# Kernel optimization log

Measured on AMD Instinct MI355X. Metric: run time of the kernel, lower is better.

## Reference

```python
import jax, jax.numpy as jnp
import numpy as np

N = 50000
E = 600000
IN1, IN2, HID, OUT = 256, 128, 128, 64


def gcn_conv(x, W, b, src, dst, n):
    """PyG GCNConv: D^{-1/2}(A+I)D^{-1/2} X W + b with self-loops."""
    h = x @ W  # [N, F_out]
    # degree including self-loop (edge weight 1)
    deg = jax.ops.segment_sum(jnp.ones_like(dst, dtype=h.dtype), dst, num_segments=n) + 1.0
    dinv = deg ** -0.5
    coef = dinv[src] * dinv[dst]  # [E]
    agg = jax.ops.segment_sum(h[src] * coef[:, None], dst, num_segments=n)
    agg = agg + h * (dinv * dinv)[:, None]  # self-loop contribution
    return agg + b


def gcn_stack(x, edge_index, Ws, bs, n):
    src, dst = edge_index[0], edge_index[1]
    x = jax.nn.relu(gcn_conv(x, Ws[0], bs[0], src, dst, n))
    return gcn_conv(x, Ws[1], bs[1], src, dst, n)


def setup_inputs() -> dict:
    key = jax.random.key(0)
    ks = jax.random.split(key, 12)
    glorot = lambda k, fi, fo: jax.random.normal(k, (fi, fo), jnp.float32) * np.sqrt(2.0 / (fi + fo))
    return {
        "x1": jax.random.normal(ks[0], (N, IN1), jnp.float32),
        "edge_index1": jax.random.randint(ks[1], (2, E), 0, N, jnp.int32),
        "x2": jax.random.normal(ks[2], (N, IN2), jnp.float32),
        "edge_index2": jax.random.randint(ks[3], (2, E), 0, N, jnp.int32),
        "W1_0": glorot(ks[4], IN1, HID), "b1_0": jnp.zeros((HID,), jnp.float32),
        "W1_1": glorot(ks[5], HID, OUT), "b1_1": jnp.zeros((OUT,), jnp.float32),
        "W2_0": glorot(ks[6], IN2, HID), "b2_0": jnp.zeros((HID,), jnp.float32),
        "W2_1": glorot(ks[7], HID, OUT), "b2_1": jnp.zeros((OUT,), jnp.float32),
    }


def reference(x1, edge_index1, x2, edge_index2,
              W1_0, b1_0, W1_1, b1_1, W2_0, b2_0, W2_1, b2_1):
    out1 = gcn_stack(x1, edge_index1, (W1_0, W1_1), (b1_0, b1_1), N)
    out2 = gcn_stack(x2, edge_index2, (W2_0, W2_1), (b2_0, b2_1), N)
    return out1, out2
```

## Files before the change

kernel.cpp:

```cpp
#include <hip/hip_runtime.h>
#include <hip/hip_bf16.h>
#include <cstdint>
#include <type_traits>

static constexpr int NN = 50000;
static constexpr int NE = 600000;
static constexpr int NB = (NN + 255) / 256;
static constexpr int CHUNK = 1024;
static constexpr int NCH = (NE + CHUNK - 1) / CHUNK;
static constexpr int CAP = 4096;

typedef __bf16 bf16;
typedef __attribute__((ext_vector_type(2))) __bf16 bf16x2;
typedef __attribute__((ext_vector_type(8))) __bf16 bf16x8;
typedef __attribute__((ext_vector_type(4))) float f32x4;

__global__ __launch_bounds__(256) void k_init(int* __restrict__ bucketcur,
                                              int* __restrict__ row_off) {
    int i = blockIdx.x * 256 + threadIdx.x;
    if (i < 2 * NB) bucketcur[i] = i * CAP;
    if (i < 2) row_off[i * (NN + 1) + NN] = NE;
}

__global__ __launch_bounds__(256) void k_binA(const int* __restrict__ srcA,
                                              const int* __restrict__ dstA,
                                              const int* __restrict__ srcB,
                                              const int* __restrict__ dstB,
                                              int* __restrict__ bucketcur,
                                              int2* __restrict__ stg) {
    __shared__ int cnt[NB];
    __shared__ int ibase[NB];
    int g = blockIdx.y;
    const int* src = g ? srcB : srcA;
    const int* dst = g ? dstB : dstA;
    int tid = threadIdx.x;
    int c0 = blockIdx.x * CHUNK;
    if (tid < NB) cnt[tid] = 0;
    __syncthreads();
    #pragma unroll
    for (int it = 0; it < CHUNK / 256; ++it) {
        int e = c0 + it * 256 + tid;
        if (e < NE) atomicAdd(&cnt[dst[e] >> 8], 1);
    }
    __syncthreads();
    if (tid < NB) {
        int c = cnt[tid];
        ibase[tid] = c ? atomicAdd(&bucketcur[g * NB + tid], c) : 0;
        cnt[tid] = 0;
    }
    __syncthreads();
    #pragma unroll
    for (int it = 0; it < CHUNK / 256; ++it) {
        int e = c0 + it * 256 + tid;
        if (e < NE) {
            int s = src[e], d = dst[e];
            int b = d >> 8;
            int p = atomicAdd(&cnt[b], 1);
            stg[(size_t)ibase[b] + p] = make_int2(s, d);
        }
    }
}

__global__ __launch_bounds__(256) void k_bucket_scan(const int* __restrict__ bucketcur,
                                                     int* __restrict__ bucket_base) {
    __shared__ int s[256];
    int g = blockIdx.x;
    int tid = threadIdx.x;
    int B = g * NB + tid;
    int v = (tid < NB) ? bucketcur[B] - B * CAP : 0;
    s[tid] = v;
    __syncthreads();
    for (int off = 1; off < 256; off <<= 1) {
        int t = (tid >= off) ? s[tid - off] : 0;
        __syncthreads();
        s[tid] += t;
        __syncthreads();
    }
    if (tid < NB) bucket_base[B] = s[tid] - v;
}

__global__ __launch_bounds__(256) void k_binB1(const int2* __restrict__ stg,
                                               const int* __restrict__ bucketcur,
                                               const int* __restrict__ bucket_base,
                                               int* __restrict__ row_off,
                                               float* __restrict__ dinv) {
    __shared__ int cnt[256];
    __shared__ int s[256];
    int g = blockIdx.y;
    int b = blockIdx.x;
    int B = g * NB + b;
    int tid = threadIdx.x;
    int node0 = b << 8;
    int nnod = min(256, NN - node0);
    cnt[tid] = 0;
    __syncthreads();
    int count = bucketcur[B] - B * CAP;
    const int2* s0 = stg + (size_t)B * CAP;
    for (int j = tid; j < count; j += 256)
        atomicAdd(&cnt[s0[j].y - node0], 1);
    __syncthreads();
    int v = cnt[tid];
    s[tid] = v;
    __syncthreads();
    for (int off = 1; off < 256; off <<= 1) {
        int t = (tid >= off) ? s[tid - off] : 0;
        __syncthreads();
        s[tid] += t;
        __syncthreads();
    }
    if (tid < nnod) {
        row_off[g * (NN + 1) + node0 + tid] = bucket_base[B] + s[tid] - v;
        dinv[(size_t)g * NN + node0 + tid] = rsqrtf((float)v + 1.0f);
    }
}

__global__ __launch_bounds__(256) void k_binB2(const int2* __restrict__ stg,
                                               const int* __restrict__ bucketcur,
                                               const int* __restrict__ row_off,
                                               const float* __restrict__ dinv,
                                               int2* __restrict__ pair) {
    __shared__ int lcur[256];
    __shared__ float ldv[256];
    int g = blockIdx.y;
    int b = blockIdx.x;
    int B = g * NB + b;
    int tid = threadIdx.x;
    int node0 = b << 8;
    int nnod = min(256, NN - node0);
    const int* ro = row_off + g * (NN + 1);
    if (tid < nnod) {
        lcur[tid] = ro[node0 + tid];
        ldv[tid] = dinv[(size_t)g * NN + node0 + tid];
    }
    __syncthreads();
    int count = bucketcur[B] - B * CAP;
    const int2* s0 = stg + (size_t)B * CAP;
    for (int j = tid; j < count; j += 256) {
        int2 sd = s0[j];
        int rel = sd.y - node0;
        int pos = atomicAdd(&lcur[rel], 1);
        float cf = dinv[(size_t)g * NN + sd.x] * ldv[rel];
        pair[(size_t)g * NE + pos] = make_int2(sd.x, __float_as_int(cf));
    }
}

__global__ __launch_bounds__(256) void k_wprep4(const float* __restrict__ WA,
                                                const float* __restrict__ WB,
                                                const float* __restrict__ WC,
                                                const float* __restrict__ WD,
                                                bf16* __restrict__ wf0,
                                                bf16* __restrict__ wf1) {
    int y = blockIdx.y;
    const float* W = (y == 0) ? WA : (y == 1) ? WB : (y == 2) ? WC : WD;
    bf16* wf = (y == 0) ? wf0 : (y == 1) ? wf0 + 256 * 128 : (y == 2) ? wf1 : wf1 + 128 * 64;
    int K = (y == 0) ? 256 : 128;
    int F = (y <= 1) ? 128 : 64;
    int i = blockIdx.x * 256 + threadIdx.x;
    if (i < K * F) {
        int k = i / F, n = i % F;
        wf[((size_t)(k >> 3) * F + n) * 8 + (k & 7)] = (bf16)W[i];
    }
}

template <int K, int F, typename AT>
__device__ __forceinline__ void gemm_body(const AT* __restrict__ X,
                                          const bf16* __restrict__ wf,
                                          bf16* __restrict__ H, int n, int bx) {
    constexpr int NT = F / 16;
    int wave = threadIdx.x >> 6;
    int lane = threadIdx.x & 63;
    int lm = lane & 15;
    int lk = lane >> 4;
    int r0 = bx * 64 + wave * 16;

    int arow = r0 + lm;
    if (arow >= n) arow = n - 1;
    const AT* xrow = X + (size_t)arow * K;

    f32x4 acc[NT] = {};

    for (int k0 = 0; k0 < K; k0 += 32) {
        bf16x8 af;
        if constexpr (std::is_same_v<AT, float>) {
            f32x4 a0 = *reinterpret_cast<const f32x4*>(xrow + k0 + lk * 8);
            f32x4 a1 = *reinterpret_cast<const f32x4*>(xrow + k0 + lk * 8 + 4);
            af[0] = (bf16)a0.x; af[1] = (bf16)a0.y; af[2] = (bf16)a0.z; af[3] = (bf16)a0.w;
            af[4] = (bf16)a1.x; af[5] = (bf16)a1.y; af[6] = (bf16)a1.z; af[7] = (bf16)a1.w;
        } else {
            af = *reinterpret_cast<const bf16x8*>(xrow + k0 + lk * 8);
        }
        const bf16* wbase = wf + ((size_t)(k0 / 8 + lk) * F) * 8;
        #pragma unroll
        for (int t = 0; t < NT; ++t) {
            bf16x8 bfg = *reinterpret_cast<const bf16x8*>(wbase + (t * 16 + lm) * 8);
            acc[t] = __builtin_amdgcn_mfma_f32_16x16x32_bf16(af, bfg, acc[t], 0, 0, 0);
        }
    }

    #pragma unroll
    for (int t = 0; t < NT; ++t) {
        #pragma unroll
        for (int i = 0; i < 4; ++i) {
            int gr = r0 + lk * 4 + i;
            if (gr < n) H[(size_t)gr * F + t * 16 + lm] = (bf16)acc[t][i];
        }
    }
}

static constexpr int GB = (NN + 63) / 64;

__global__ __launch_bounds__(256) void gemm_l1(const float* __restrict__ x1,
                                               const float* __restrict__ x2,
                                               const bf16* __restrict__ wf0,
                                               bf16* __restrict__ h) {
    int bx = blockIdx.x;
    if (bx < GB)
        gemm_body<256, 128, float>(x1, wf0, h, NN, bx);
    else
        gemm_body<128, 128, float>(x2, wf0 + 256 * 128, h + (size_t)NN * 128, NN, bx - GB);
}

__global__ __launch_bounds__(256) void gemm_l2(const bf16* __restrict__ a,
                                               const bf16* __restrict__ wf1,
                                               bf16* __restrict__ h2) {
    int bx = blockIdx.x;
    int g = (bx >= GB);
    gemm_body<128, 64, bf16>(a + (size_t)g * NN * 128, wf1 + g * 128 * 64,
                             h2 + (size_t)g * NN * 64, NN, bx - g * GB);
}

__global__ __launch_bounds__(256) void agg128_2(const bf16* __restrict__ hb,
                                                const int* __restrict__ row_off,
                                                const int2* __restrict__ pairb,
                                                const float* __restrict__ dinv,
                                                const float* __restrict__ biasA,
                                                const float* __restrict__ biasB,
                                                bf16* __restrict__ ab) {
    int wid = blockIdx.x * 4 + (threadIdx.x >> 6);
    if (wid >= 2 * NN) return;
    int g = (wid >= NN);
    int node = wid - g * NN;
    int lane = threadIdx.x & 63;

    const bf16* h = hb + (size_t)g * NN * 128;
    const int2* pair = pairb + (size_t)g * NE;
    const int* ro = row_off + g * (NN + 1);
    const float* bias = g ? biasB : biasA;

    int f = lane * 2;
    float di = dinv[g * NN + node];
    int beg = ro[node];
    int end = ro[node + 1];

    float a0 = 0.f, a1 = 0.f;

    auto edge1 = [&](int2 p) {
        float c = __int_as_float(p.y);
        bf16x2 v = *reinterpret_cast<const bf16x2*>(&h[(size_t)p.x * 128 + f]);
        a0 = fmaf((float)v[0], c, a0); a1 = fmaf((float)v[1], c, a1);
    };
    auto edge2 = [&](int4 q) {
        float cA = __int_as_float(q.y), cB = __int_as_float(q.w);
        bf16x2 vA = *reinterpret_cast<const bf16x2*>(&h[(size_t)q.x * 128 + f]);
        bf16x2 vB = *reinterpret_cast<const bf16x2*>(&h[(size_t)q.z * 128 + f]);
        a0 = fmaf((float)vA[0], cA, a0); a1 = fmaf((float)vA[1], cA, a1);
        a0 = fmaf((float)vB[0], cB, a0); a1 = fmaf((float)vB[1], cB, a1);
    };

    int j = beg;
    if ((j & 1) && j < end) { edge1(pair[j]); ++j; }
    for (; j + 7 < end; j += 8) {
        int4 q0 = *reinterpret_cast<const int4*>(&pair[j]);
        int4 q1 = *reinterpret_cast<const int4*>(&pair[j + 2]);
        int4 q2 = *reinterpret_cast<const int4*>(&pair[j + 4]);
        int4 q3 = *reinterpret_cast<const int4*>(&pair[j + 6]);
        edge2(q0); edge2(q1); edge2(q2); edge2(q3);
    }
    for (; j + 1 < end; j += 2) {
        int4 q = *reinterpret_cast<const int4*>(&pair[j]);
        edge2(q);
    }
    if (j < end) edge1(pair[j]);

    bf16x2 hv = *reinterpret_cast<const bf16x2*>(&h[(size_t)node * 128 + f]);
    float sc = di * di;
    a0 = fmaf((float)hv[0], sc, a0) + bias[f];
    a1 = fmaf((float)hv[1], sc, a1) + bias[f + 1];
    a0 = fmaxf(a0, 0.f);
    a1 = fmaxf(a1, 0.f);

    bf16x2 r;
    r[0] = (bf16)a0; r[1] = (bf16)a1;
    *reinterpret_cast<bf16x2*>(&ab[((size_t)g * NN + node) * 128 + f]) = r;
}

__global__ __launch_bounds__(256) void agg64_2(const bf16* __restrict__ h2b,
                                               const int* __restrict__ row_off,
                                               const int2* __restrict__ pairb,
                                               const float* __restrict__ dinv,
                                               const float* __restrict__ biasA,
                                               const float* __restrict__ biasB,
                                               float* __restrict__ outb) {
    int wid = blockIdx.x * 4 + (threadIdx.x >> 6);
    if (wid >= 2 * NN) return;
    int g = (wid >= NN);
    int node = wid - g * NN;
    int lane = threadIdx.x & 63;

    const bf16* h = h2b + (size_t)g * NN * 64;
    const int2* pair = pairb + (size_t)g * NE;
    const int* ro = row_off + g * (NN + 1);
    const float* bias = g ? biasB : biasA;
    float* out = outb + (size_t)g * NN * 64;

    int half = lane >> 5;
    int f = (lane & 31) * 2;
    float di = dinv[(size_t)g * NN + node];
    int beg = ro[node];
    int end = ro[node + 1];

    float a0 = 0.f, a1 = 0.f;

    auto edge = [&](int2 p) {
        float c = __int_as_float(p.y);
        bf16x2 v = *reinterpret_cast<const bf16x2*>(&h[(size_t)p.x * 64 + f]);
        a0 = fmaf((float)v[0], c, a0); a1 = fmaf((float)v[1], c, a1);
    };

    int j = beg;
    for (; j + 7 < end; j += 8) {
        int2 p0 = pair[j + half], p1 = pair[j + 2 + half];
        int2 p2 = pair[j + 4 + half], p3 = pair[j + 6 + half];
        edge(p0); edge(p1); edge(p2); edge(p3);
    }
    for (; j + 1 < end; j += 2) edge(pair[j + half]);
    if (j < end && half == 0) edge(pair[j]);

    a0 += __shfl_xor(a0, 32);
    a1 += __shfl_xor(a1, 32);

    bf16x2 hv = *reinterpret_cast<const bf16x2*>(&h[(size_t)node * 64 + f]);
    float sc = di * di;
    a0 = fmaf((float)hv[0], sc, a0) + bias[f];
    a1 = fmaf((float)hv[1], sc, a1) + bias[f + 1];

    if (half == 0) {
        out[(size_t)node * 64 + f] = a0;
        out[(size_t)node * 64 + f + 1] = a1;
    }
}

extern "C" void kernel_launch(void* const* d_in, const int* in_sizes, int n_in,
                              void* d_out, int out_size, void* d_ws, size_t ws_size,
                              hipStream_t stream) {
    const float* x1 = (const float*)d_in[0];
    const int* ei1 = (const int*)d_in[1];
    const float* x2 = (const float*)d_in[2];
    const int* ei2 = (const int*)d_in[3];
    const float* W1_0 = (const float*)d_in[4];
    const float* b1_0 = (const float*)d_in[5];
    const float* W1_1 = (const float*)d_in[6];
    const float* b1_1 = (const float*)d_in[7];
    const float* W2_0 = (const float*)d_in[8];
    const float* b2_0 = (const float*)d_in[9];
    const float* W2_1 = (const float*)d_in[10];
    const float* b2_1 = (const float*)d_in[11];

    float* out = (float*)d_out;

    char* ws = (char*)d_ws;
    size_t off = 0;
    auto alloc = [&](size_t bytes) {
        size_t o = off;
        off = (off + bytes + 255) & ~(size_t)255;
        return o;
    };
    bf16* h = (bf16*)(ws + alloc((size_t)2 * NN * 128 * 2));
    size_t r2 = (size_t)2 * NB * CAP * 8;
    char* region2 = ws + alloc(r2);
    int2* stg = (int2*)region2;
    bf16* h2 = (bf16*)region2;
    bf16* a = (bf16*)(ws + alloc((size_t)2 * NN * 128 * 2));
    int2* pair = (int2*)(ws + alloc((size_t)2 * NE * 8));
    int* row_off = (int*)(ws + alloc((size_t)2 * (NN + 1) * 4));
    float* dinv = (float*)(ws + alloc((size_t)2 * NN * 4));
    int* bucketcur = (int*)(ws + alloc((size_t)2 * NB * 4));
    int* bucket_base = (int*)(ws + alloc((size_t)2 * NB * 4));
    bf16* wf0 = (bf16*)(ws + alloc((size_t)2 * 256 * 128 * 2));
    bf16* wf1 = (bf16*)(ws + alloc((size_t)2 * 128 * 64 * 2));

    const int* srcA = ei1, *dstA = ei1 + NE;
    const int* srcB = ei2, *dstB = ei2 + NE;

    k_init<<<(2 * NB + 255) / 256, 256, 0, stream>>>(bucketcur, row_off);
    k_wprep4<<<dim3(128, 4), 256, 0, stream>>>(W1_0, W2_0, W1_1, W2_1, wf0, wf1);
    k_binA<<<dim3(NCH, 2), 256, 0, stream>>>(srcA, dstA, srcB, dstB, bucketcur, stg);
    k_bucket_scan<<<2, 256, 0, stream>>>(bucketcur, bucket_base);
    k_binB1<<<dim3(NB, 2), 256, 0, stream>>>(stg, bucketcur, bucket_base, row_off, dinv);
    k_binB2<<<dim3(NB, 2), 256, 0, stream>>>(stg, bucketcur, row_off, dinv, pair);

    gemm_l1<<<2 * GB, 256, 0, stream>>>(x1, x2, wf0, h);
    agg128_2<<<(2 * NN + 3) / 4, 256, 0, stream>>>(h, row_off, pair, dinv, b1_0, b2_0, a);
    gemm_l2<<<2 * GB, 256, 0, stream>>>(a, wf1, h2);
    agg64_2<<<(2 * NN + 3) / 4, 256, 0, stream>>>(h2, row_off, pair, dinv, b1_1, b2_1, out);
}
```

Before: 201.7 us.

## Split edges across half-waves in agg128, use nontemporal pair loads, fuse init kernel

The 128-wide aggregation now gives each half-wave alternating edges, with 4 features per lane and 8-byte gathers, and combines the two halves with a cross-half shuffle. This mirrors the existing agg64 scheme and halves the per-lane edge count. Edge pair loads in both aggregation kernels use nontemporal hints so streaming metadata is kept out of cache in favour of the gathered features. The separate init kernel is folded into the weight-prep kernel as an extra grid row, saving one launch. The costs are shuffle overhead and only half the lanes writing the output.

```diff
diff --git a/kernel.cpp b/kernel.cpp
--- a/kernel.cpp
+++ b/kernel.cpp
@@ -12,15 +12,11 @@
 
 typedef __bf16 bf16;
 typedef __attribute__((ext_vector_type(2))) __bf16 bf16x2;
+typedef __attribute__((ext_vector_type(4))) __bf16 bf16x4;
 typedef __attribute__((ext_vector_type(8))) __bf16 bf16x8;
 typedef __attribute__((ext_vector_type(4))) float f32x4;
-
-__global__ __launch_bounds__(256) void k_init(int* __restrict__ bucketcur,
-                                              int* __restrict__ row_off) {
-    int i = blockIdx.x * 256 + threadIdx.x;
-    if (i < 2 * NB) bucketcur[i] = i * CAP;
-    if (i < 2) row_off[i * (NN + 1) + NN] = NE;
-}
+typedef __attribute__((ext_vector_type(2))) int i32x2;
+typedef __attribute__((ext_vector_type(4))) int i32x4;
 
 __global__ __launch_bounds__(256) void k_binA(const int* __restrict__ srcA,
                                               const int* __restrict__ dstA,
@@ -149,13 +145,20 @@
                                                 const float* __restrict__ WC,
                                                 const float* __restrict__ WD,
                                                 bf16* __restrict__ wf0,
-                                                bf16* __restrict__ wf1) {
+                                                bf16* __restrict__ wf1,
+                                                int* __restrict__ bucketcur,
+                                                int* __restrict__ row_off) {
     int y = blockIdx.y;
+    int i = blockIdx.x * 256 + threadIdx.x;
+    if (y == 4) {
+        if (i < 2 * NB) bucketcur[i] = i * CAP;
+        if (i < 2) row_off[i * (NN + 1) + NN] = NE;
+        return;
+    }
     const float* W = (y == 0) ? WA : (y == 1) ? WB : (y == 2) ? WC : WD;
     bf16* wf = (y == 0) ? wf0 : (y == 1) ? wf0 + 256 * 128 : (y == 2) ? wf1 : wf1 + 128 * 64;
     int K = (y == 0) ? 256 : 128;
     int F = (y <= 1) ? 128 : 64;
-    int i = blockIdx.x * 256 + threadIdx.x;
     if (i < K * F) {
         int k = i / F, n = i % F;
         wf[((size_t)(k >> 3) * F + n) * 8 + (k & 7)] = (bf16)W[i];
@@ -241,57 +244,67 @@
     int g = (wid >= NN);
     int node = wid - g * NN;
     int lane = threadIdx.x & 63;
+    int half = lane >> 5;
+    int f = (lane & 31) * 4;
 
     const bf16* h = hb + (size_t)g * NN * 128;
     const int2* pair = pairb + (size_t)g * NE;
     const int* ro = row_off + g * (NN + 1);
     const float* bias = g ? biasB : biasA;
 
-    int f = lane * 2;
     float di = dinv[g * NN + node];
     int beg = ro[node];
     int end = ro[node + 1];
 
-    float a0 = 0.f, a1 = 0.f;
-
-    auto edge1 = [&](int2 p) {
-        float c = __int_as_float(p.y);
-        bf16x2 v = *reinterpret_cast<const bf16x2*>(&h[(size_t)p.x * 128 + f]);
+    float a0 = 0.f, a1 = 0.f, a2 = 0.f, a3 = 0.f;
+
+    auto edge = [&](int s, float c) {
+        bf16x4 v = *reinterpret_cast<const bf16x4*>(&h[(size_t)s * 128 + f]);
         a0 = fmaf((float)v[0], c, a0); a1 = fmaf((float)v[1], c, a1);
+        a2 = fmaf((float)v[2], c, a2); a3 = fmaf((float)v[3], c, a3);
     };
-    auto edge2 = [&](int4 q) {
-        float cA = __int_as_float(q.y), cB = __int_as_float(q.w);
-        bf16x2 vA = *reinterpret_cast<const bf16x2*>(&h[(size_t)q.x * 128 + f]);
-        bf16x2 vB = *reinterpret_cast<const bf16x2*>(&h[(size_t)q.z * 128 + f]);
-        a0 = fmaf((float)vA[0], cA, a0); a1 = fmaf((float)vA[1], cA, a1);
-        a0 = fmaf((float)vB[0], cB, a0); a1 = fmaf((float)vB[1], cB, a1);
+    auto edge2 = [&](i32x4 q) {
+        int s = half ? q[2] : q[0];
+        float c = __int_as_float(half ? q[3] : q[1]);
+        edge(s, c);
     };
 
     int j = beg;
-    if ((j & 1) && j < end) { edge1(pair[j]); ++j; }
+    if ((j & 1) && j < end) {
+        if (half == 0) { int2 p = pair[j]; edge(p.x, __int_as_float(p.y)); }
+        ++j;
+    }
     for (; j + 7 < end; j += 8) {
-        int4 q0 = *reinterpret_cast<const int4*>(&pair[j]);
-        int4 q1 = *reinterpret_cast<const int4*>(&pair[j + 2]);
-        int4 q2 = *reinterpret_cast<const int4*>(&pair[j + 4]);
-        int4 q3 = *reinterpret_cast<const int4*>(&pair[j + 6]);
+        i32x4 q0 = __builtin_nontemporal_load(reinterpret_cast<const i32x4*>(&pair[j]));
+        i32x4 q1 = __builtin_nontemporal_load(reinterpret_cast<const i32x4*>(&pair[j + 2]));
+        i32x4 q2 = __builtin_nontemporal_load(reinterpret_cast<const i32x4*>(&pair[j + 4]));
+        i32x4 q3 = __builtin_nontemporal_load(reinterpret_cast<const i32x4*>(&pair[j + 6]));
         edge2(q0); edge2(q1); edge2(q2); edge2(q3);
     }
     for (; j + 1 < end; j += 2) {
-        int4 q = *reinterpret_cast<const int4*>(&pair[j]);
+        i32x4 q = __builtin_nontemporal_load(reinterpret_cast<const i32x4*>(&pair[j]));
         edge2(q);
     }
-    if (j < end) edge1(pair[j]);
-
-    bf16x2 hv = *reinterpret_cast<const bf16x2*>(&h[(size_t)node * 128 + f]);
+    if (j < end && half == 0) { int2 p = pair[j]; edge(p.x, __int_as_float(p.y)); }
+
+    a0 += __shfl_xor(a0, 32);
+    a1 += __shfl_xor(a1, 32);
+    a2 += __shfl_xor(a2, 32);
+    a3 += __shfl_xor(a3, 32);
+
+    bf16x4 hv = *reinterpret_cast<const bf16x4*>(&h[(size_t)node * 128 + f]);
+    f32x4 bv = *reinterpret_cast<const f32x4*>(&bias[f]);
     float sc = di * di;
-    a0 = fmaf((float)hv[0], sc, a0) + bias[f];
-    a1 = fmaf((float)hv[1], sc, a1) + bias[f + 1];
-    a0 = fmaxf(a0, 0.f);
-    a1 = fmaxf(a1, 0.f);
-
-    bf16x2 r;
-    r[0] = (bf16)a0; r[1] = (bf16)a1;
-    *reinterpret_cast<bf16x2*>(&ab[((size_t)g * NN + node) * 128 + f]) = r;
+    a0 = fmaxf(fmaf((float)hv[0], sc, a0) + bv.x, 0.f);
+    a1 = fmaxf(fmaf((float)hv[1], sc, a1) + bv.y, 0.f);
+    a2 = fmaxf(fmaf((float)hv[2], sc, a2) + bv.z, 0.f);
+    a3 = fmaxf(fmaf((float)hv[3], sc, a3) + bv.w, 0.f);
+
+    if (half == 0) {
+        bf16x4 r;
+        r[0] = (bf16)a0; r[1] = (bf16)a1; r[2] = (bf16)a2; r[3] = (bf16)a3;
+        *reinterpret_cast<bf16x4*>(&ab[((size_t)g * NN + node) * 128 + f]) = r;
+    }
 }
 
 __global__ __launch_bounds__(256) void agg64_2(const bf16* __restrict__ h2b,
@@ -321,20 +334,29 @@
 
     float a0 = 0.f, a1 = 0.f;
 
-    auto edge = [&](int2 p) {
-        float c = __int_as_float(p.y);
-        bf16x2 v = *reinterpret_cast<const bf16x2*>(&h[(size_t)p.x * 64 + f]);
+    auto edge = [&](i32x2 p) {
+        float c = __int_as_float(p[1]);
+        bf16x2 v = *reinterpret_cast<const bf16x2*>(&h[(size_t)p[0] * 64 + f]);
         a0 = fmaf((float)v[0], c, a0); a1 = fmaf((float)v[1], c, a1);
     };
 
     int j = beg;
     for (; j + 7 < end; j += 8) {
-        int2 p0 = pair[j + half], p1 = pair[j + 2 + half];
-        int2 p2 = pair[j + 4 + half], p3 = pair[j + 6 + half];
+        i32x2 p0 = __builtin_nontemporal_load(reinterpret_cast<const i32x2*>(&pair[j + half]));
+        i32x2 p1 = __builtin_nontemporal_load(reinterpret_cast<const i32x2*>(&pair[j + 2 + half]));
+        i32x2 p2 = __builtin_nontemporal_load(reinterpret_cast<const i32x2*>(&pair[j + 4 + half]));
+        i32x2 p3 = __builtin_nontemporal_load(reinterpret_cast<const i32x2*>(&pair[j + 6 + half]));
         edge(p0); edge(p1); edge(p2); edge(p3);
     }
-    for (; j + 1 < end; j += 2) edge(pair[j + half]);
-    if (j < end && half == 0) edge(pair[j]);
+    for (; j + 1 < end; j += 2) {
+        i32x2 p = __builtin_nontemporal_load(reinterpret_cast<const i32x2*>(&pair[j + half]));
+        edge(p);
+    }
+    if (j < end && half == 0) {
+        int2 p = pair[j];
+        i32x2 q; q[0] = p.x; q[1] = p.y;
+        edge(q);
+    }
 
     a0 += __shfl_xor(a0, 32);
     a1 += __shfl_xor(a1, 32);
@@ -392,8 +414,8 @@
     const int* srcA = ei1, *dstA = ei1 + NE;
     const int* srcB = ei2, *dstB = ei2 + NE;
 
-    k_init<<<(2 * NB + 255) / 256, 256, 0, stream>>>(bucketcur, row_off);
-    k_wprep4<<<dim3(128, 4), 256, 0, stream>>>(W1_0, W2_0, W1_1, W2_1, wf0, wf1);
+    k_wprep4<<<dim3(128, 5), 256, 0, stream>>>(W1_0, W2_0, W1_1, W2_1, wf0, wf1,
+                                               bucketcur, row_off);
     k_binA<<<dim3(NCH, 2), 256, 0, stream>>>(srcA, dstA, srcB, dstB, bucketcur, stg);
     k_bucket_scan<<<2, 256, 0, stream>>>(bucketcur, bucket_base);
     k_binB1<<<dim3(NB, 2), 256, 0, stream>>>(stg, bucketcur, bucket_base, row_off, dinv);
```

Result: slower. 221.5 us (+9.8%).
